# Performance work log

Measured on AMD Instinct MI355X. Metric: run time of the kernel, lower is better.

## Reference

```python
import jax, jax.numpy as jnp
import numpy as np

V, C, BLK = 32000, 512, 2048
B, T = 4, 2048
EPS = 1e-5


def _layernorm(x, g, b):
    mu = jnp.mean(x, axis=-1, keepdims=True)
    var = jnp.mean(jnp.square(x - mu), axis=-1, keepdims=True)
    return (x - mu) * jax.lax.rsqrt(var + EPS) * g + b


def setup_inputs() -> dict:
    key = jax.random.key(0)
    ks = jax.random.split(key, 16)
    s = 0.02
    return {
        "idx": jax.random.randint(ks[0], (B, T), 0, V),
        "targets": jax.random.randint(ks[1], (B, T), 0, V),
        "tok_emb": jax.random.normal(ks[2], (V, C), jnp.float32) * s,
        "pos_emb": jax.random.normal(ks[3], (BLK, C), jnp.float32) * s,
        "Wk": jax.random.normal(ks[4], (C, C), jnp.float32) * s,
        "Wq": jax.random.normal(ks[5], (C, C), jnp.float32) * s,
        "Wv": jax.random.normal(ks[6], (C, C), jnp.float32) * s,
        "W1": jax.random.normal(ks[7], (4 * C, C), jnp.float32) * s,
        "b1": jnp.zeros((4 * C,), jnp.float32),
        "W2": jax.random.normal(ks[8], (C, 4 * C), jnp.float32) * s,
        "b2": jnp.zeros((C,), jnp.float32),
        "g1": jnp.ones((C,), jnp.float32),
        "beta1": jnp.zeros((C,), jnp.float32),
        "g2": jnp.ones((C,), jnp.float32),
        "beta2": jnp.zeros((C,), jnp.float32),
        "Wlm": jax.random.normal(ks[9], (V, C), jnp.float32) * s,
        "blm": jnp.zeros((V,), jnp.float32),
    }


def reference(idx, targets, tok_emb, pos_emb, Wk, Wq, Wv, W1, b1, W2, b2,
              g1, beta1, g2, beta2, Wlm, blm):
    # embeddings
    x = tok_emb[idx] + pos_emb[:T]  # [B,T,C]
    # single-head causal self-attention (dropout = identity, eval mode)
    h = _layernorm(x, g1, beta1)
    q = jnp.einsum('btc,dc->btd', h, Wq)
    k = jnp.einsum('btc,dc->btd', h, Wk)
    v = jnp.einsum('btc,dc->btd', h, Wv)
    wei = jnp.einsum('btd,bsd->bts', q, k) * (C ** -0.5)  # [B,T,T]
    mask = jnp.tril(jnp.ones((T, T), bool))
    wei = jnp.where(mask, wei, -jnp.inf)
    wei = jax.nn.softmax(wei, axis=-1)
    x = x + jnp.einsum('bts,bsd->btd', wei, v)
    # FFN
    h2 = _layernorm(x, g2, beta2)
    ff = jax.nn.relu(jnp.einsum('btc,fc->btf', h2, W1) + b1)
    x = x + jnp.einsum('btf,cf->btc', ff, W2) + b2
    # lm head + cross-entropy
    logits = (jnp.einsum('btc,vc->btv', x, Wlm) + blm).reshape(B * T, V)
    logp = jax.nn.log_softmax(logits, axis=-1)
    loss = -jnp.mean(jnp.take_along_axis(logp, targets.reshape(-1, 1), axis=1))
    return logits, loss
```

## Files before the change

### kernel.cpp

```cpp
#include <hip/hip_runtime.h>

typedef __bf16 bf16;
typedef __bf16 bf16x8 __attribute__((ext_vector_type(8)));
typedef float  f32x4  __attribute__((ext_vector_type(4)));

#define NB 4
#define NT 2048
#define NC 512
#define NV 32000
#define NROWS (NB*NT)
#define NCHUNK 250
#define LNEPS 1e-5f
#define SMEM_B 131072

static __device__ __forceinline__ void load_lds16(const bf16* g, char* l) {
  __builtin_amdgcn_global_load_lds(
      (const __attribute__((address_space(1))) void*)g,
      (__attribute__((address_space(3))) void*)l, 16, 0, 0);
}

static __device__ __forceinline__ void bar() {
  asm volatile("" ::: "memory");
  __builtin_amdgcn_s_barrier();
  asm volatile("" ::: "memory");
}

__global__ __launch_bounds__(256)
void cvt_kernel(const float* __restrict__ in, bf16* __restrict__ out, int n8) {
  long i = (long)blockIdx.x * 256 + threadIdx.x;
  long stride = (long)gridDim.x * 256;
  for (; i < n8; i += stride) {
    const float* p = in + i * 8;
    f32x4 a = *(const f32x4*)p;
    f32x4 b = *(const f32x4*)(p + 4);
    bf16x8 o;
    o[0]=(bf16)a.x; o[1]=(bf16)a.y; o[2]=(bf16)a.z; o[3]=(bf16)a.w;
    o[4]=(bf16)b.x; o[5]=(bf16)b.y; o[6]=(bf16)b.z; o[7]=(bf16)b.w;
    *(bf16x8*)(out + i*8) = o;
  }
}

__global__ __launch_bounds__(64)
void embed_ln_kernel(const int* __restrict__ idx, const float* __restrict__ tok,
                     const float* __restrict__ pos, const float* __restrict__ gw,
                     const float* __restrict__ bw,
                     float* __restrict__ x0, bf16* __restrict__ h1) {
  int row = blockIdx.x;
  int t = row & (NT-1);
  int id = idx[row];
  int lane = threadIdx.x;
  const float* tr = tok + (long)id*NC + lane*8;
  const float* pr = pos + (long)t*NC + lane*8;
  f32x4 a0 = *(const f32x4*)tr, a1 = *(const f32x4*)(tr+4);
  f32x4 p0 = *(const f32x4*)pr, p1 = *(const f32x4*)(pr+4);
  f32x4 r0 = a0 + p0, r1 = a1 + p1;
  float* o = x0 + (long)row*NC + lane*8;
  *(f32x4*)o = r0; *(f32x4*)(o+4) = r1;
  float v[8] = {r0.x,r0.y,r0.z,r0.w,r1.x,r1.y,r1.z,r1.w};
  float s = 0.f;
  #pragma unroll
  for (int j=0;j<8;++j) s += v[j];
  #pragma unroll
  for (int m=32;m>=1;m>>=1) s += __shfl_xor(s, m);
  float mu = s * (1.f/NC);
  float sq = 0.f;
  #pragma unroll
  for (int j=0;j<8;++j) { v[j] -= mu; sq += v[j]*v[j]; }
  #pragma unroll
  for (int m=32;m>=1;m>>=1) sq += __shfl_xor(sq, m);
  float rs = rsqrtf(sq * (1.f/NC) + LNEPS);
  const float* gp = gw + lane*8;
  const float* bp = bw + lane*8;
  f32x4 g0 = *(const f32x4*)gp, g1 = *(const f32x4*)(gp+4);
  f32x4 b0 = *(const f32x4*)bp, b1 = *(const f32x4*)(bp+4);
  float gg[8] = {g0.x,g0.y,g0.z,g0.w,g1.x,g1.y,g1.z,g1.w};
  float bb[8] = {b0.x,b0.y,b0.z,b0.w,b1.x,b1.y,b1.z,b1.w};
  bf16x8 oo;
  #pragma unroll
  for (int j=0;j<8;++j) oo[j] = (bf16)(v[j]*rs*gg[j] + bb[j]);
  *(bf16x8*)(h1 + (long)row*NC + lane*8) = oo;
}

__global__ __launch_bounds__(256)
void transpose_kernel(const bf16* __restrict__ v, long ldv, bf16* __restrict__ vt) {
  __shared__ bf16 tile[64][66];
  int b = blockIdx.z;
  int t0 = blockIdx.x*64, c0 = blockIdx.y*64;
  int tid = threadIdx.x;
  int r = tid >> 2, ch = (tid & 3) * 16;
  const bf16* src = v + ((long)b*NT + t0 + r)*ldv + c0 + ch;
  #pragma unroll
  for (int i=0;i<16;++i) tile[r][ch+i] = src[i];
  __syncthreads();
  bf16x8 o0, o1;
  #pragma unroll
  for (int i=0;i<8;++i) o0[i] = tile[ch+i][r];
  #pragma unroll
  for (int i=0;i<8;++i) o1[i] = tile[ch+8+i][r];
  bf16* dst = vt + ((long)b*NC + c0 + r)*NT + t0 + ch;
  *(bf16x8*)dst = o0;
  *(bf16x8*)(dst+8) = o1;
}

__global__ __launch_bounds__(256)
void softmax_kernel(float* __restrict__ S) {
  const int row = blockIdx.x;
  const int t = row & (NT-1);
  const int tid = threadIdx.x;
  float* sr = S + (long)row*NT;
  bf16* pr = (bf16*)S + (long)row*(2*NT);
  const float scale = 0.044194173824159216f;
  f32x4 v0 = *(const f32x4*)(sr + tid*8);
  f32x4 v1 = *(const f32x4*)(sr + tid*8 + 4);
  float v[8] = {v0.x,v0.y,v0.z,v0.w,v1.x,v1.y,v1.z,v1.w};
  int cb = tid*8;
  float mx = -1e30f;
  #pragma unroll
  for (int j=0;j<8;++j) {
    v[j] = (cb + j <= t) ? v[j]*scale : -1e30f;
    mx = fmaxf(mx, v[j]);
  }
  __shared__ float redm[4];
  #pragma unroll
  for (int m=32;m>=1;m>>=1) mx = fmaxf(mx, __shfl_xor(mx, m));
  if ((tid & 63) == 0) redm[tid>>6] = mx;
  __syncthreads();
  mx = fmaxf(fmaxf(redm[0],redm[1]), fmaxf(redm[2],redm[3]));
  float e[8]; float s = 0.f;
  #pragma unroll
  for (int j=0;j<8;++j) { e[j] = (cb + j <= t) ? __expf(v[j]-mx) : 0.f; s += e[j]; }
  __shared__ float reds[4];
  #pragma unroll
  for (int m=32;m>=1;m>>=1) s += __shfl_xor(s, m);
  if ((tid & 63) == 0) reds[tid>>6] = s;
  __syncthreads();
  s = reds[0]+reds[1]+reds[2]+reds[3];
  float inv = 1.f/s;
  bf16x8 o;
  #pragma unroll
  for (int j=0;j<8;++j) o[j] = (bf16)(e[j]*inv);
  *(bf16x8*)(pr + cb) = o;
}

enum { EPI_F32=0, EPI_BF16=1, EPI_BIAS_RELU_BF16=2, EPI_BIAS_RES_BF16=3, EPI_RES_F32=4 };

template<int EPI, bool CAUSAL=false, bool SWAP=false, bool KCHUNK=false>
__global__ __launch_bounds__(512,2)
void gemm256(const bf16* __restrict__ A, const bf16* __restrict__ B, int nkt,
             long lda, long ldb, long sAb, long sBb,
             float* __restrict__ outf, bf16* __restrict__ outb, long ldo, long sOb,
             const float* __restrict__ bias,
             const float* __restrict__ res, long ldr, long sRb) {
  extern __shared__ char smem[];
  int bn, bm;
  if constexpr (SWAP) { bm = blockIdx.x; bn = blockIdx.y; }
  else               { bn = blockIdx.x; bm = blockIdx.y; }
  const int bz = blockIdx.z;
  if constexpr (CAUSAL) { if (bn > bm) return; }
  int nkt_eff = nkt;
  int bzAB = bz;
  long kOff = 0;
  if constexpr (KCHUNK) {
    int c = bz >> 2; bzAB = bz & 3;
    int lim = (bm+1)*4 - c*8;
    if (lim <= 0) return;
    if (lim < nkt_eff) nkt_eff = lim;
    kOff = (long)c*512;
  }

  const int tid = threadIdx.x;
  const int wid = tid >> 6, lane = tid & 63;
  const int wr = wid >> 2, wc = wid & 3;
  const int l15 = lane & 15, g = lane >> 4;

  const bf16* Ab = A + (long)bzAB*sAb + kOff + (long)bm*256*lda;
  const bf16* Bb = B + (long)bzAB*sBb + kOff + (long)bn*256*ldb;

  const int colsw = 8 * ((tid & 7) ^ ((tid >> 3) & 7));
  const bf16* A0 = Ab + (long)(tid >> 3)*lda + colsw;
  const bf16* B0 = Bb + (long)(tid >> 3)*ldb + colsw;

  auto stage = [&](int ab, int t, int h, int slot) {
    char* dst = smem + slot*65536 + ab*32768 + h*16384 + wid*1024;
    const bf16* s0 = (ab ? B0 : A0) + (long)(h*128)*(ab ? ldb : lda) + (long)t*64;
    load_lds16(s0, dst);
    load_lds16(s0 + 64*(ab ? ldb : lda), dst + 8192);
  };

  const char* sm = smem;
  auto aLoad = [&](int slot, int m, int kk) -> bf16x8 {
    int row = m*16 + l15;
    int b = row*128 + ((kk*64 + g*16) ^ ((row & 7) << 4));
    return *(const bf16x8*)(sm + slot*65536 + wr*16384 + b);
  };
  auto bLoad = [&](int slot, int n, int kk) -> bf16x8 {
    int row = (wc & 1)*64 + n*16 + l15;
    int b = row*128 + ((kk*64 + g*16) ^ ((row & 7) << 4));
    return *(const bf16x8*)(sm + slot*65536 + 32768 + (wc >> 1)*16384 + b);
  };

  f32x4 acc[8][4] = {};

  stage(0, 0, 0, 0);
  stage(0, 0, 1, 0);
  stage(1, 0, 0, 0);
  stage(1, 0, 1, 0);
  stage(0, 1, 0, 1);
  asm volatile("s_waitcnt vmcnt(2)" ::: "memory");
  bar();

  const int niter = nkt_eff >> 1;
  for (int it = 0; it < niter; ++it) {
    const int t0 = 2*it, t1 = 2*it + 1;
    const int tn0 = (t0+2 < nkt_eff) ? t0+2 : nkt_eff-1;
    const int tn1 = (t1+2 < nkt_eff) ? t1+2 : nkt_eff-1;
    bf16x8 a0[4][2], a1[4][2], b0[2][2], b1[2][2];

    #pragma unroll
    for (int m=0;m<4;++m) { a0[m][0]=aLoad(0,m,0); a0[m][1]=aLoad(0,m,1); }
    #pragma unroll
    for (int n=0;n<2;++n) { b0[n][0]=bLoad(0,n,0); b0[n][1]=bLoad(0,n,1); }
    stage(0, t1, 1, 1);
    bar();
    __builtin_amdgcn_s_setprio(1);
    #pragma unroll
    for (int m=0;m<4;++m)
      #pragma unroll
      for (int n=0;n<2;++n) {
        acc[m][n] = __builtin_amdgcn_mfma_f32_16x16x32_bf16(a0[m][0], b0[n][0], acc[m][n],0,0,0);
        acc[m][n] = __builtin_amdgcn_mfma_f32_16x16x32_bf16(a0[m][1], b0[n][1], acc[m][n],0,0,0);
      }
    __builtin_amdgcn_s_setprio(0);
    bar();
    #pragma unroll
    for (int n=0;n<2;++n) { b1[n][0]=bLoad(0,n+2,0); b1[n][1]=bLoad(0,n+2,1); }
    stage(1, t1, 0, 1);
    bar();
    __builtin_amdgcn_s_setprio(1);
    #pragma unroll
    for (int m=0;m<4;++m)
      #pragma unroll
      for (int n=0;n<2;++n) {
        acc[m][n+2] = __builtin_amdgcn_mfma_f32_16x16x32_bf16(a0[m][0], b1[n][0], acc[m][n+2],0,0,0);
        acc[m][n+2] = __builtin_amdgcn_mfma_f32_16x16x32_bf16(a0[m][1], b1[n][1], acc[m][n+2],0,0,0);
      }
    __builtin_amdgcn_s_setprio(0);
    bar();
    #pragma unroll
    for (int m=0;m<4;++m) { a1[m][0]=aLoad(0,m+4,0); a1[m][1]=aLoad(0,m+4,1); }
    stage(1, t1, 1, 1);
    bar();
    __builtin_amdgcn_s_setprio(1);
    #pragma unroll
    for (int m=0;m<4;++m)
      #pragma unroll
      for (int n=0;n<2;++n) {
        acc[m+4][n+2] = __builtin_amdgcn_mfma_f32_16x16x32_bf16(a1[m][0], b1[n][0], acc[m+4][n+2],0,0,0);
        acc[m+4][n+2] = __builtin_amdgcn_mfma_f32_16x16x32_bf16(a1[m][1], b1[n][1], acc[m+4][n+2],0,0,0);
      }
    __builtin_amdgcn_s_setprio(0);
    bar();
    stage(0, tn0, 0, 0);
    asm volatile("s_waitcnt vmcnt(2)" ::: "memory");
    bar();
    __builtin_amdgcn_s_setprio(1);
    #pragma unroll
    for (int m=0;m<4;++m)
      #pragma unroll
      for (int n=0;n<2;++n) {
        acc[m+4][n] = __builtin_amdgcn_mfma_f32_16x16x32_bf16(a1[m][0], b0[n][0], acc[m+4][n],0,0,0);
        acc[m+4][n] = __builtin_amdgcn_mfma_f32_16x16x32_bf16(a1[m][1], b0[n][1], acc[m+4][n],0,0,0);
      }
    __builtin_amdgcn_s_setprio(0);
    bar();
    #pragma unroll
    for (int m=0;m<4;++m) { a0[m][0]=aLoad(1,m,0); a0[m][1]=aLoad(1,m,1); }
    #pragma unroll
    for (int n=0;n<2;++n) { b0[n][0]=bLoad(1,n,0); b0[n][1]=bLoad(1,n,1); }
    stage(0, tn0, 1, 0);
    bar();
    __builtin_amdgcn_s_setprio(1);
    #pragma unroll
    for (int m=0;m<4;++m)
      #pragma unroll
      for (int n=0;n<2;++n) {
        acc[m][n] = __builtin_amdgcn_mfma_f32_16x16x32_bf16(a0[m][0], b0[n][0], acc[m][n],0,0,0);
        acc[m][n] = __builtin_amdgcn_mfma_f32_16x16x32_bf16(a0[m][1], b0[n][1], acc[m][n],0,0,0);
      }
    __builtin_amdgcn_s_setprio(0);
    bar();
    #pragma unroll
    for (int n=0;n<2;++n) { b1[n][0]=bLoad(1,n+2,0); b1[n][1]=bLoad(1,n+2,1); }
    stage(1, tn0, 0, 0);
    bar();
    __builtin_amdgcn_s_setprio(1);
    #pragma unroll
    for (int m=0;m<4;++m)
      #pragma unroll
      for (int n=0;n<2;++n) {
        acc[m][n+2] = __builtin_amdgcn_mfma_f32_16x16x32_bf16(a0[m][0], b1[n][0], acc[m][n+2],0,0,0);
        acc[m][n+2] = __builtin_amdgcn_mfma_f32_16x16x32_bf16(a0[m][1], b1[n][1], acc[m][n+2],0,0,0);
      }
    __builtin_amdgcn_s_setprio(0);
    bar();
    #pragma unroll
    for (int m=0;m<4;++m) { a1[m][0]=aLoad(1,m+4,0); a1[m][1]=aLoad(1,m+4,1); }
    stage(1, tn0, 1, 0);
    bar();
    __builtin_amdgcn_s_setprio(1);
    #pragma unroll
    for (int m=0;m<4;++m)
      #pragma unroll
      for (int n=0;n<2;++n) {
        acc[m+4][n+2] = __builtin_amdgcn_mfma_f32_16x16x32_bf16(a1[m][0], b1[n][0], acc[m+4][n+2],0,0,0);
        acc[m+4][n+2] = __builtin_amdgcn_mfma_f32_16x16x32_bf16(a1[m][1], b1[n][1], acc[m+4][n+2],0,0,0);
      }
    __builtin_amdgcn_s_setprio(0);
    bar();
    stage(0, tn1, 0, 1);
    asm volatile("s_waitcnt vmcnt(2)" ::: "memory");
    bar();
    __builtin_amdgcn_s_setprio(1);
    #pragma unroll
    for (int m=0;m<4;++m)
      #pragma unroll
      for (int n=0;n<2;++n) {
        acc[m+4][n] = __builtin_amdgcn_mfma_f32_16x16x32_bf16(a1[m][0], b0[n][0], acc[m+4][n],0,0,0);
        acc[m+4][n] = __builtin_amdgcn_mfma_f32_16x16x32_bf16(a1[m][1], b0[n][1], acc[m+4][n],0,0,0);
      }
    __builtin_amdgcn_s_setprio(0);
    bar();
  }

  const long rowbase = (long)bm*256 + wr*128;
  const long colbase = (long)bn*256 + wc*64;

  #pragma unroll
  for (int m=0;m<8;++m)
    #pragma unroll
    for (int n=0;n<4;++n) {
      long c = colbase + n*16 + l15;
      #pragma unroll
      for (int q_=0;q_<4;++q_) {
        long rr = rowbase + m*16 + g*4 + q_;
        float v = acc[m][n][q_];
        if constexpr (EPI == EPI_F32) {
          outf[(long)bz*sOb + rr*ldo + c] = v;
        } else if constexpr (EPI == EPI_BF16) {
          outb[(long)bz*sOb + rr*ldo + c] = (bf16)v;
        } else if constexpr (EPI == EPI_BIAS_RELU_BF16) {
          outb[rr*ldo + c] = (bf16)fmaxf(v + bias[c], 0.f);
        } else if constexpr (EPI == EPI_BIAS_RES_BF16) {
          outb[rr*ldo + c] = (bf16)(v + bias[c] + res[rr*ldr + c]);
        } else if constexpr (EPI == EPI_RES_F32) {
          outf[(long)bz*sOb + rr*ldo + c] = v + res[(long)bz*sRb + rr*ldr + c];
        }
      }
    }
}

__global__ __launch_bounds__(256)
void lmhead128(const bf16* __restrict__ A, const bf16* __restrict__ B,
               const float* __restrict__ bias, float* __restrict__ outf,
               float* __restrict__ pmax, float* __restrict__ psum) {
  __shared__ char As[8192];
  __shared__ char Bs[8192];
  const int bm = blockIdx.x, bn = blockIdx.y;
  const int tid = threadIdx.x;
  const int wid = tid >> 6, lane = tid & 63;
  const int wr = wid >> 1, wc = wid & 1;
  const int l15 = lane & 15, g = lane >> 4;

  const int p0 = tid, p1 = tid + 256;
  const int r0_ = 2*(p0>>3) + ((p0>>2)&1), c0_ = 8*((p0&3) ^ ((p0>>3)&3));
  const int r1_ = 2*(p1>>3) + ((p1>>2)&1), c1_ = 8*((p1&3) ^ ((p1>>3)&3));
  const bf16* A00 = A + ((long)bm*128 + r0_)*NC + c0_;
  const bf16* A01 = A + ((long)bm*128 + r1_)*NC + c1_;
  const bf16* B00 = B + ((long)bn*128 + r0_)*NC + c0_;
  const bf16* B01 = B + ((long)bn*128 + r1_)*NC + c1_;
  char* dA0 = As + wid*1024;
  char* dA1 = As + 4096 + wid*1024;
  char* dB0 = Bs + wid*1024;
  char* dB1 = Bs + 4096 + wid*1024;

  f32x4 acc[4][4] = {};

  for (int kt = 0; kt < 16; ++kt) {
    __syncthreads();
    load_lds16(A00 + kt*32, dA0);
    load_lds16(A01 + kt*32, dA1);
    load_lds16(B00 + kt*32, dB0);
    load_lds16(B01 + kt*32, dB1);
    __syncthreads();
    bf16x8 af[4], bf_[4];
    #pragma unroll
    for (int m=0;m<4;++m) {
      int R = wr*64 + m*16 + l15;
      af[m] = *(const bf16x8*)(As + (R>>1)*128 + (R&1)*64 + ((g ^ ((R>>1)&3))<<4));
    }
    #pragma unroll
    for (int n=0;n<4;++n) {
      int R = wc*64 + n*16 + l15;
      bf_[n] = *(const bf16x8*)(Bs + (R>>1)*128 + (R&1)*64 + ((g ^ ((R>>1)&3))<<4));
    }
    #pragma unroll
    for (int m=0;m<4;++m)
      #pragma unroll
      for (int n=0;n<4;++n)
        acc[m][n] = __builtin_amdgcn_mfma_f32_16x16x32_bf16(af[m], bf_[n], acc[m][n],0,0,0);
  }

  const long rowb = (long)bm*128;
  const long colb = (long)bn*128;
  #pragma unroll
  for (int m=0;m<4;++m)
    #pragma unroll
    for (int n=0;n<4;++n) {
      long c = colb + wc*64 + n*16 + l15;
      float bv = bias[c];
      #pragma unroll
      for (int q=0;q<4;++q) {
        acc[m][n][q] += bv;
        long rr = rowb + wr*64 + m*16 + g*4 + q;
        __builtin_nontemporal_store(acc[m][n][q], &outf[rr*NV + c]);
      }
    }
  __syncthreads();
  float* redm = (float*)As;
  float* reds = redm + 256;
  #pragma unroll
  for (int m=0;m<4;++m)
    #pragma unroll
    for (int q=0;q<4;++q) {
      float mx = fmaxf(fmaxf(acc[m][0][q], acc[m][1][q]),
                       fmaxf(acc[m][2][q], acc[m][3][q]));
      #pragma unroll
      for (int msk=8;msk>=1;msk>>=1) mx = fmaxf(mx, __shfl_xor(mx, msk));
      float se = 0.f;
      #pragma unroll
      for (int n=0;n<4;++n) se += __expf(acc[m][n][q] - mx);
      #pragma unroll
      for (int msk=8;msk>=1;msk>>=1) se += __shfl_xor(se, msk);
      if (l15 == 0) {
        int R = wr*64 + m*16 + g*4 + q;
        redm[wc*128 + R] = mx;
        reds[wc*128 + R] = se;
      }
    }
  __syncthreads();
  if (tid < 128) {
    float m0 = redm[tid], m1 = redm[128+tid];
    float M = fmaxf(m0, m1);
    float Sv = reds[tid]*__expf(m0-M) + reds[128+tid]*__expf(m1-M);
    long row = rowb + tid;
    pmax[row*NCHUNK + bn] = M;
    psum[row*NCHUNK + bn] = Sv;
  }
}

__global__ __launch_bounds__(64)
void pv_combine_ln_kernel(const float* __restrict__ part, const float* __restrict__ x0,
                          const float* __restrict__ gw, const float* __restrict__ bw,
                          float* __restrict__ x1, bf16* __restrict__ h2) {
  int row = blockIdx.x;
  int b = row >> 11, t = row & (NT-1);
  int lane = threadIdx.x;
  int nC = (t >> 9) + 1;
  const float* xr = x0 + (long)row*NC + lane*8;
  f32x4 a0 = *(const f32x4*)xr, a1 = *(const f32x4*)(xr+4);
  for (int c = 0; c < nC; ++c) {
    const float* pr = part + ((long)(c*4 + b)*NT + t)*NC + lane*8;
    a0 += *(const f32x4*)pr; a1 += *(const f32x4*)(pr+4);
  }
  float* o = x1 + (long)row*NC + lane*8;
  *(f32x4*)o = a0; *(f32x4*)(o+4) = a1;
  float v[8] = {a0.x,a0.y,a0.z,a0.w,a1.x,a1.y,a1.z,a1.w};
  float s = 0.f;
  #pragma unroll
  for (int j=0;j<8;++j) s += v[j];
  #pragma unroll
  for (int m=32;m>=1;m>>=1) s += __shfl_xor(s, m);
  float mu = s * (1.f/NC);
  float sq = 0.f;
  #pragma unroll
  for (int j=0;j<8;++j) { v[j] -= mu; sq += v[j]*v[j]; }
  #pragma unroll
  for (int m=32;m>=1;m>>=1) sq += __shfl_xor(sq, m);
  float rs = rsqrtf(sq * (1.f/NC) + LNEPS);
  const float* gp = gw + lane*8;
  const float* bp = bw + lane*8;
  f32x4 g0 = *(const f32x4*)gp, g1 = *(const f32x4*)(gp+4);
  f32x4 b0 = *(const f32x4*)bp, b1 = *(const f32x4*)(bp+4);
  float gg[8] = {g0.x,g0.y,g0.z,g0.w,g1.x,g1.y,g1.z,g1.w};
  float bb[8] = {b0.x,b0.y,b0.z,b0.w,b1.x,b1.y,b1.z,b1.w};
  bf16x8 oo;
  #pragma unroll
  for (int j=0;j<8;++j) oo[j] = (bf16)(v[j]*rs*gg[j] + bb[j]);
  *(bf16x8*)(h2 + (long)row*NC + lane*8) = oo;
}

__global__ __launch_bounds__(64)
void ffn2_combine_kernel(const float* __restrict__ part, const float* __restrict__ x1,
                         const float* __restrict__ b2, bf16* __restrict__ x2) {
  int row = blockIdx.x;
  int lane = threadIdx.x;
  const float* xr = x1 + (long)row*NC + lane*8;
  f32x4 a0 = *(const f32x4*)xr, a1 = *(const f32x4*)(xr+4);
  const float* br = b2 + lane*8;
  a0 += *(const f32x4*)br; a1 += *(const f32x4*)(br+4);
  #pragma unroll
  for (int z = 0; z < 4; ++z) {
    const float* pr = part + ((long)z*NROWS + row)*NC + lane*8;
    a0 += *(const f32x4*)pr; a1 += *(const f32x4*)(pr+4);
  }
  bf16x8 o;
  o[0]=(bf16)a0.x; o[1]=(bf16)a0.y; o[2]=(bf16)a0.z; o[3]=(bf16)a0.w;
  o[4]=(bf16)a1.x; o[5]=(bf16)a1.y; o[6]=(bf16)a1.z; o[7]=(bf16)a1.w;
  *(bf16x8*)(x2 + (long)row*NC + lane*8) = o;
}

__global__ __launch_bounds__(256)
void loss1_kernel(const float* __restrict__ pmax, const float* __restrict__ psum,
                  const float* __restrict__ logits, const int* __restrict__ targets,
                  float* __restrict__ rowloss) {
  int row = blockIdx.x;
  int tid = threadIdx.x;
  int lane = tid & 63, wv = tid >> 6;
  float cm = (tid < NCHUNK) ? pmax[(long)row*NCHUNK + tid] : -1e30f;
  float cs = (tid < NCHUNK) ? psum[(long)row*NCHUNK + tid] : 0.f;
  float mx = cm;
  #pragma unroll
  for (int m=32;m>=1;m>>=1) mx = fmaxf(mx, __shfl_xor(mx, m));
  __shared__ float rm[4];
  if (lane == 0) rm[wv] = mx;
  __syncthreads();
  float M = fmaxf(fmaxf(rm[0],rm[1]), fmaxf(rm[2],rm[3]));
  float sc = cs * __expf(cm - M);
  #pragma unroll
  for (int m=32;m>=1;m>>=1) sc += __shfl_xor(sc, m);
  __shared__ float rs_[4];
  if (lane == 0) rs_[wv] = sc;
  __syncthreads();
  if (tid == 0) {
    float Sv = rs_[0]+rs_[1]+rs_[2]+rs_[3];
    float lse = M + logf(Sv);
    int tgt = targets[row];
    float lg = logits[(long)row*NV + tgt];
    rowloss[row] = lse - lg;
  }
}

__global__ __launch_bounds__(256)
void loss2_kernel(const float* __restrict__ rowloss, float* __restrict__ out) {
  int tid = threadIdx.x;
  float s = 0.f;
  for (int i = tid; i < NROWS; i += 256) s += rowloss[i];
  #pragma unroll
  for (int m=32;m>=1;m>>=1) s += __shfl_xor(s, m);
  __shared__ float rs_[4];
  if ((tid & 63) == 0) rs_[tid>>6] = s;
  __syncthreads();
  if (tid == 0) out[0] = (rs_[0]+rs_[1]+rs_[2]+rs_[3]) * (1.f/NROWS);
}

extern "C" void kernel_launch(void* const* d_in, const int* in_sizes, int n_in,
                              void* d_out, int out_size, void* d_ws, size_t ws_size,
                              hipStream_t stream) {
  const int*   idx  = (const int*)d_in[0];
  const int*   tgt  = (const int*)d_in[1];
  const float* tok  = (const float*)d_in[2];
  const float* pos  = (const float*)d_in[3];
  const float* Wk   = (const float*)d_in[4];
  const float* Wq   = (const float*)d_in[5];
  const float* Wv   = (const float*)d_in[6];
  const float* W1   = (const float*)d_in[7];
  const float* b1   = (const float*)d_in[8];
  const float* W2   = (const float*)d_in[9];
  const float* b2   = (const float*)d_in[10];
  const float* g1   = (const float*)d_in[11];
  const float* be1  = (const float*)d_in[12];
  const float* g2   = (const float*)d_in[13];
  const float* be2  = (const float*)d_in[14];
  const float* Wlm  = (const float*)d_in[15];
  const float* blm  = (const float*)d_in[16];

  float* logits = (float*)d_out;
  float* loss   = logits + (long)NROWS*NV;

  char* w = (char*)d_ws;
  auto alloc = [&](size_t bytes) -> char* {
    char* p = w; w += (bytes + 255) & ~(size_t)255; return p;
  };
  bf16* wqkvb = (bf16*)alloc((size_t)3*NC*NC*2);
  bf16* w1b   = (bf16*)alloc((size_t)4*NC*NC*2);
  bf16* w2b   = (bf16*)alloc((size_t)4*NC*NC*2);
  bf16* wlmb  = (bf16*)alloc((size_t)NV*NC*2);
  float* x0   = (float*)alloc((size_t)NROWS*NC*4);
  bf16* h1b   = (bf16*)alloc((size_t)NROWS*NC*2);
  bf16* qkvb  = (bf16*)alloc((size_t)NROWS*3*NC*2);
  bf16* vtb   = (bf16*)alloc((size_t)NROWS*NC*2);
  float* Sb   = (float*)alloc((size_t)NB*NT*NT*4);
  float* pvp  = (float*)alloc((size_t)16*NT*NC*4);
  float* x1   = (float*)alloc((size_t)NROWS*NC*4);
  bf16* h2b   = (bf16*)alloc((size_t)NROWS*NC*2);
  bf16* ffb   = (bf16*)alloc((size_t)NROWS*4*NC*2);
  bf16* x2b   = (bf16*)alloc((size_t)NROWS*NC*2);
  float* pmax = (float*)alloc((size_t)NROWS*NCHUNK*4);
  float* psum = (float*)alloc((size_t)NROWS*NCHUNK*4);
  float* rowloss = (float*)alloc((size_t)NROWS*4);
  float* ff2p = Sb;

  hipFuncSetAttribute((const void*)gemm256<EPI_BF16,false,false,false>,
                      hipFuncAttributeMaxDynamicSharedMemorySize, SMEM_B);
  hipFuncSetAttribute((const void*)gemm256<EPI_F32,true,false,false>,
                      hipFuncAttributeMaxDynamicSharedMemorySize, SMEM_B);
  hipFuncSetAttribute((const void*)gemm256<EPI_F32,false,false,true>,
                      hipFuncAttributeMaxDynamicSharedMemorySize, SMEM_B);
  hipFuncSetAttribute((const void*)gemm256<EPI_F32,false,false,false>,
                      hipFuncAttributeMaxDynamicSharedMemorySize, SMEM_B);
  hipFuncSetAttribute((const void*)gemm256<EPI_BIAS_RELU_BF16,false,true,false>,
                      hipFuncAttributeMaxDynamicSharedMemorySize, SMEM_B);

  auto cvt = [&](const float* in, bf16* out, long n) {
    int n8 = (int)(n/8);
    int blocks = (n8 + 255)/256; if (blocks > 2048) blocks = 2048;
    cvt_kernel<<<blocks, 256, 0, stream>>>(in, out, n8);
  };
  cvt(Wq, wqkvb, (long)NC*NC);
  cvt(Wk, wqkvb + (long)NC*NC, (long)NC*NC);
  cvt(Wv, wqkvb + (long)2*NC*NC, (long)NC*NC);
  cvt(W1, w1b, (long)4*NC*NC);
  cvt(W2, w2b, (long)4*NC*NC);
  cvt(Wlm, wlmb, (long)NV*NC);

  embed_ln_kernel<<<NROWS, 64, 0, stream>>>(idx, tok, pos, g1, be1, x0, h1b);

  gemm256<EPI_BF16><<<dim3(6,32,1), 512, SMEM_B, stream>>>(
      h1b, wqkvb, 8, NC, NC, 0, 0, nullptr, qkvb, 3*NC, 0,
      nullptr, nullptr, 0, 0);

  transpose_kernel<<<dim3(NT/64, NC/64, NB), 256, 0, stream>>>(qkvb + 2*NC, 3*NC, vtb);

  gemm256<EPI_F32,true><<<dim3(8,8,NB), 512, SMEM_B, stream>>>(
      qkvb, qkvb + NC, 8, 3*NC, 3*NC, (long)NT*3*NC, (long)NT*3*NC,
      Sb, nullptr, NT, (long)NT*NT,
      nullptr, nullptr, 0, 0);

  softmax_kernel<<<NROWS, 256, 0, stream>>>(Sb);

  gemm256<EPI_F32,false,false,true><<<dim3(2,8,16), 512, SMEM_B, stream>>>(
      (const bf16*)Sb, vtb, 8, 2*NT, NT, (long)NT*2*NT, (long)NC*NT,
      pvp, nullptr, NC, (long)NT*NC,
      nullptr, nullptr, 0, 0);

  pv_combine_ln_kernel<<<NROWS, 64, 0, stream>>>(pvp, x0, g2, be2, x1, h2b);

  gemm256<EPI_BIAS_RELU_BF16,false,true><<<dim3(32,8,1), 512, SMEM_B, stream>>>(
      h2b, w1b, 8, NC, NC, 0, 0, nullptr, ffb, 4*NC, 0,
      b1, nullptr, 0, 0);

  gemm256<EPI_F32><<<dim3(2,32,4), 512, SMEM_B, stream>>>(
      ffb, w2b, 8, 4*NC, 4*NC, 512, 512,
      ff2p, nullptr, NC, (long)NROWS*NC,
      nullptr, nullptr, 0, 0);

  ffn2_combine_kernel<<<NROWS, 64, 0, stream>>>(ff2p, x1, b2, x2b);

  lmhead128<<<dim3(64, NCHUNK), 256, 0, stream>>>(x2b, wlmb, blm, logits, pmax, psum);

  loss1_kernel<<<NROWS, 256, 0, stream>>>(pmax, psum, logits, tgt, rowloss);
  loss2_kernel<<<1, 256, 0, stream>>>(rowloss, loss);
}
```

Baseline: 756.2 us.

## Double-buffer LM-head GEMM tiles with BK=64 and async LDS prefetch

Rewrites the LM-head GEMM main loop to use two 32KB LDS slots with a K-tile of 64 instead of 32. The next tile is prefetched via global_load_lds while MFMAs run on the current one, and the loop has one barrier per iteration instead of two. MFMA sections also raise wave priority. The cost is 64KB of LDS per block, which may lower occupancy for a kernel that also writes a large fp32 logits output.

```diff
diff --git a/kernel.cpp b/kernel.cpp
--- a/kernel.cpp
+++ b/kernel.cpp
@@ -363,51 +363,67 @@
 void lmhead128(const bf16* __restrict__ A, const bf16* __restrict__ B,
                const float* __restrict__ bias, float* __restrict__ outf,
                float* __restrict__ pmax, float* __restrict__ psum) {
-  __shared__ char As[8192];
-  __shared__ char Bs[8192];
+  __shared__ char sm[65536];
   const int bm = blockIdx.x, bn = blockIdx.y;
   const int tid = threadIdx.x;
   const int wid = tid >> 6, lane = tid & 63;
   const int wr = wid >> 1, wc = wid & 1;
   const int l15 = lane & 15, g = lane >> 4;
 
-  const int p0 = tid, p1 = tid + 256;
-  const int r0_ = 2*(p0>>3) + ((p0>>2)&1), c0_ = 8*((p0&3) ^ ((p0>>3)&3));
-  const int r1_ = 2*(p1>>3) + ((p1>>2)&1), c1_ = 8*((p1&3) ^ ((p1>>3)&3));
-  const bf16* A00 = A + ((long)bm*128 + r0_)*NC + c0_;
-  const bf16* A01 = A + ((long)bm*128 + r1_)*NC + c1_;
-  const bf16* B00 = B + ((long)bn*128 + r0_)*NC + c0_;
-  const bf16* B01 = B + ((long)bn*128 + r1_)*NC + c1_;
-  char* dA0 = As + wid*1024;
-  char* dA1 = As + 4096 + wid*1024;
-  char* dB0 = Bs + wid*1024;
-  char* dB1 = Bs + 4096 + wid*1024;
+  const int rr_ = tid >> 3;
+  const int colsw = 8 * ((tid & 7) ^ (rr_ & 7));
+  const bf16* Abase = A + ((long)bm*128 + rr_)*NC + colsw;
+  const bf16* Bbase = B + ((long)bn*128 + rr_)*NC + colsw;
+
+  auto stage = [&](int kt, int slot) {
+    char* dA = sm + slot*32768 + wid*1024;
+    char* dB = sm + slot*32768 + 16384 + wid*1024;
+    const bf16* a = Abase + kt*64;
+    const bf16* b = Bbase + kt*64;
+    #pragma unroll
+    for (int j = 0; j < 4; ++j) {
+      load_lds16(a + (long)j*32*NC, dA + j*4096);
+      load_lds16(b + (long)j*32*NC, dB + j*4096);
+    }
+  };
+
+  auto aLoad = [&](int slot, int m, int kk) -> bf16x8 {
+    int R = wr*64 + m*16 + l15;
+    int s = kk*4 + g;
+    return *(const bf16x8*)(sm + slot*32768 + R*128 + ((s ^ (R & 7)) << 4));
+  };
+  auto bLoad = [&](int slot, int n, int kk) -> bf16x8 {
+    int R = wc*64 + n*16 + l15;
+    int s = kk*4 + g;
+    return *(const bf16x8*)(sm + slot*32768 + 16384 + R*128 + ((s ^ (R & 7)) << 4));
+  };
 
   f32x4 acc[4][4] = {};
 
-  for (int kt = 0; kt < 16; ++kt) {
-    __syncthreads();
-    load_lds16(A00 + kt*32, dA0);
-    load_lds16(A01 + kt*32, dA1);
-    load_lds16(B00 + kt*32, dB0);
-    load_lds16(B01 + kt*32, dB1);
-    __syncthreads();
-    bf16x8 af[4], bf_[4];
-    #pragma unroll
-    for (int m=0;m<4;++m) {
-      int R = wr*64 + m*16 + l15;
-      af[m] = *(const bf16x8*)(As + (R>>1)*128 + (R&1)*64 + ((g ^ ((R>>1)&3))<<4));
-    }
-    #pragma unroll
-    for (int n=0;n<4;++n) {
-      int R = wc*64 + n*16 + l15;
-      bf_[n] = *(const bf16x8*)(Bs + (R>>1)*128 + (R&1)*64 + ((g ^ ((R>>1)&3))<<4));
-    }
-    #pragma unroll
-    for (int m=0;m<4;++m)
-      #pragma unroll
-      for (int n=0;n<4;++n)
-        acc[m][n] = __builtin_amdgcn_mfma_f32_16x16x32_bf16(af[m], bf_[n], acc[m][n],0,0,0);
+  stage(0, 0);
+  asm volatile("s_waitcnt vmcnt(0)" ::: "memory");
+  bar();
+
+  int cur = 0;
+  for (int kt = 0; kt < 8; ++kt) {
+    if (kt < 7) stage(kt + 1, cur ^ 1);
+    bf16x8 af[4][2], bf_[4][2];
+    #pragma unroll
+    for (int m=0;m<4;++m) { af[m][0]=aLoad(cur,m,0); af[m][1]=aLoad(cur,m,1); }
+    #pragma unroll
+    for (int n=0;n<4;++n) { bf_[n][0]=bLoad(cur,n,0); bf_[n][1]=bLoad(cur,n,1); }
+    __builtin_amdgcn_s_setprio(1);
+    #pragma unroll
+    for (int m=0;m<4;++m)
+      #pragma unroll
+      for (int n=0;n<4;++n) {
+        acc[m][n] = __builtin_amdgcn_mfma_f32_16x16x32_bf16(af[m][0], bf_[n][0], acc[m][n],0,0,0);
+        acc[m][n] = __builtin_amdgcn_mfma_f32_16x16x32_bf16(af[m][1], bf_[n][1], acc[m][n],0,0,0);
+      }
+    __builtin_amdgcn_s_setprio(0);
+    asm volatile("s_waitcnt vmcnt(0)" ::: "memory");
+    bar();
+    cur ^= 1;
   }
 
   const long rowb = (long)bm*128;
@@ -426,7 +442,7 @@
       }
     }
   __syncthreads();
-  float* redm = (float*)As;
+  float* redm = (float*)sm;
   float* reds = redm + 256;
   #pragma unroll
   for (int m=0;m<4;++m)
```

After: 809.5 us. 1.07x slower.

## Double-buffer LM-head LDS loads and write per-wave softmax partials directly

Applied to the files above, without the earlier changes.

The LM-head GEMM kernel now uses two LDS stages, prefetching the next K tile while MFMAs run on the current one, and raises MFMA priority with setprio. It drops the block-level LDS reduction of row max and sum and instead writes per-half-tile partials directly, doubling NCHUNK to 500. The logits store moves after the reduction, and loss1 is widened to 512 threads to combine the extra partials. This trades more partial-sum traffic and 32KB of LDS per block for fewer barriers and overlapped loads in the dominant GEMM.

```diff
diff --git a/kernel.cpp b/kernel.cpp
--- a/kernel.cpp
+++ b/kernel.cpp
@@ -9,7 +9,7 @@
 #define NC 512
 #define NV 32000
 #define NROWS (NB*NT)
-#define NCHUNK 250
+#define NCHUNK 500
 #define LNEPS 1e-5f
 #define SMEM_B 131072
 
@@ -359,12 +359,11 @@
     }
 }
 
-__global__ __launch_bounds__(256)
+__global__ __launch_bounds__(256,4)
 void lmhead128(const bf16* __restrict__ A, const bf16* __restrict__ B,
                const float* __restrict__ bias, float* __restrict__ outf,
                float* __restrict__ pmax, float* __restrict__ psum) {
-  __shared__ char As[8192];
-  __shared__ char Bs[8192];
+  __shared__ char sm[32768];
   const int bm = blockIdx.x, bn = blockIdx.y;
   const int tid = threadIdx.x;
   const int wid = tid >> 6, lane = tid & 63;
@@ -378,56 +377,62 @@
   const bf16* A01 = A + ((long)bm*128 + r1_)*NC + c1_;
   const bf16* B00 = B + ((long)bn*128 + r0_)*NC + c0_;
   const bf16* B01 = B + ((long)bn*128 + r1_)*NC + c1_;
-  char* dA0 = As + wid*1024;
-  char* dA1 = As + 4096 + wid*1024;
-  char* dB0 = Bs + wid*1024;
-  char* dB1 = Bs + 4096 + wid*1024;
+
+  auto stage = [&](int kt, int slot) {
+    char* base = sm + slot*16384 + wid*1024;
+    load_lds16(A00 + kt*32, base);
+    load_lds16(A01 + kt*32, base + 4096);
+    load_lds16(B00 + kt*32, base + 8192);
+    load_lds16(B01 + kt*32, base + 12288);
+  };
+
+  auto aLoad = [&](int slot, int m) -> bf16x8 {
+    int R = wr*64 + m*16 + l15;
+    return *(const bf16x8*)(sm + slot*16384 + (R>>1)*128 + (R&1)*64
+                            + ((g ^ ((R>>1)&3)) << 4));
+  };
+  auto bLoad = [&](int slot, int n) -> bf16x8 {
+    int R = wc*64 + n*16 + l15;
+    return *(const bf16x8*)(sm + slot*16384 + 8192 + (R>>1)*128 + (R&1)*64
+                            + ((g ^ ((R>>1)&3)) << 4));
+  };
 
   f32x4 acc[4][4] = {};
 
+  stage(0, 0);
+  asm volatile("s_waitcnt vmcnt(0)" ::: "memory");
+  bar();
+
+  int cur = 0;
   for (int kt = 0; kt < 16; ++kt) {
-    __syncthreads();
-    load_lds16(A00 + kt*32, dA0);
-    load_lds16(A01 + kt*32, dA1);
-    load_lds16(B00 + kt*32, dB0);
-    load_lds16(B01 + kt*32, dB1);
-    __syncthreads();
+    if (kt < 15) stage(kt + 1, cur ^ 1);
     bf16x8 af[4], bf_[4];
     #pragma unroll
-    for (int m=0;m<4;++m) {
-      int R = wr*64 + m*16 + l15;
-      af[m] = *(const bf16x8*)(As + (R>>1)*128 + (R&1)*64 + ((g ^ ((R>>1)&3))<<4));
-    }
-    #pragma unroll
-    for (int n=0;n<4;++n) {
-      int R = wc*64 + n*16 + l15;
-      bf_[n] = *(const bf16x8*)(Bs + (R>>1)*128 + (R&1)*64 + ((g ^ ((R>>1)&3))<<4));
-    }
+    for (int m=0;m<4;++m) af[m] = aLoad(cur, m);
+    #pragma unroll
+    for (int n=0;n<4;++n) bf_[n] = bLoad(cur, n);
+    __builtin_amdgcn_s_setprio(1);
     #pragma unroll
     for (int m=0;m<4;++m)
       #pragma unroll
       for (int n=0;n<4;++n)
         acc[m][n] = __builtin_amdgcn_mfma_f32_16x16x32_bf16(af[m], bf_[n], acc[m][n],0,0,0);
+    __builtin_amdgcn_s_setprio(0);
+    asm volatile("s_waitcnt vmcnt(0)" ::: "memory");
+    bar();
+    cur ^= 1;
   }
 
   const long rowb = (long)bm*128;
   const long colb = (long)bn*128;
   #pragma unroll
-  for (int m=0;m<4;++m)
-    #pragma unroll
-    for (int n=0;n<4;++n) {
-      long c = colb + wc*64 + n*16 + l15;
-      float bv = bias[c];
-      #pragma unroll
-      for (int q=0;q<4;++q) {
-        acc[m][n][q] += bv;
-        long rr = rowb + wr*64 + m*16 + g*4 + q;
-        __builtin_nontemporal_store(acc[m][n][q], &outf[rr*NV + c]);
-      }
-    }
-  __syncthreads();
-  float* redm = (float*)As;
-  float* reds = redm + 256;
+  for (int n=0;n<4;++n) {
+    float bv = bias[colb + wc*64 + n*16 + l15];
+    #pragma unroll
+    for (int m=0;m<4;++m)
+      #pragma unroll
+      for (int q=0;q<4;++q) acc[m][n][q] += bv;
+  }
   #pragma unroll
   for (int m=0;m<4;++m)
     #pragma unroll
@@ -442,20 +447,22 @@
       #pragma unroll
       for (int msk=8;msk>=1;msk>>=1) se += __shfl_xor(se, msk);
       if (l15 == 0) {
-        int R = wr*64 + m*16 + g*4 + q;
-        redm[wc*128 + R] = mx;
-        reds[wc*128 + R] = se;
+        long row = rowb + wr*64 + m*16 + g*4 + q;
+        pmax[row*NCHUNK + bn*2 + wc] = mx;
+        psum[row*NCHUNK + bn*2 + wc] = se;
       }
     }
-  __syncthreads();
-  if (tid < 128) {
-    float m0 = redm[tid], m1 = redm[128+tid];
-    float M = fmaxf(m0, m1);
-    float Sv = reds[tid]*__expf(m0-M) + reds[128+tid]*__expf(m1-M);
-    long row = rowb + tid;
-    pmax[row*NCHUNK + bn] = M;
-    psum[row*NCHUNK + bn] = Sv;
-  }
+  #pragma unroll
+  for (int m=0;m<4;++m)
+    #pragma unroll
+    for (int n=0;n<4;++n) {
+      long c = colb + wc*64 + n*16 + l15;
+      #pragma unroll
+      for (int q=0;q<4;++q) {
+        long rr = rowb + wr*64 + m*16 + g*4 + q;
+        __builtin_nontemporal_store(acc[m][n][q], &outf[rr*NV + c]);
+      }
+    }
 }
 
 __global__ __launch_bounds__(64)
@@ -519,7 +526,7 @@
   *(bf16x8*)(x2 + (long)row*NC + lane*8) = o;
 }
 
-__global__ __launch_bounds__(256)
+__global__ __launch_bounds__(512)
 void loss1_kernel(const float* __restrict__ pmax, const float* __restrict__ psum,
                   const float* __restrict__ logits, const int* __restrict__ targets,
                   float* __restrict__ rowloss) {
@@ -531,18 +538,22 @@
   float mx = cm;
   #pragma unroll
   for (int m=32;m>=1;m>>=1) mx = fmaxf(mx, __shfl_xor(mx, m));
-  __shared__ float rm[4];
+  __shared__ float rm[8];
   if (lane == 0) rm[wv] = mx;
   __syncthreads();
-  float M = fmaxf(fmaxf(rm[0],rm[1]), fmaxf(rm[2],rm[3]));
+  float M = rm[0];
+  #pragma unroll
+  for (int i=1;i<8;++i) M = fmaxf(M, rm[i]);
   float sc = cs * __expf(cm - M);
   #pragma unroll
   for (int m=32;m>=1;m>>=1) sc += __shfl_xor(sc, m);
-  __shared__ float rs_[4];
+  __shared__ float rs_[8];
   if (lane == 0) rs_[wv] = sc;
   __syncthreads();
   if (tid == 0) {
-    float Sv = rs_[0]+rs_[1]+rs_[2]+rs_[3];
+    float Sv = 0.f;
+    #pragma unroll
+    for (int i=0;i<8;++i) Sv += rs_[i];
     float lse = M + logf(Sv);
     int tgt = targets[row];
     float lg = logits[(long)row*NV + tgt];
@@ -666,8 +677,8 @@
 
   ffn2_combine_kernel<<<NROWS, 64, 0, stream>>>(ff2p, x1, b2, x2b);
 
-  lmhead128<<<dim3(64, NCHUNK), 256, 0, stream>>>(x2b, wlmb, blm, logits, pmax, psum);
-
-  loss1_kernel<<<NROWS, 256, 0, stream>>>(pmax, psum, logits, tgt, rowloss);
+  lmhead128<<<dim3(64, NV/128), 256, 0, stream>>>(x2b, wlmb, blm, logits, pmax, psum);
+
+  loss1_kernel<<<NROWS, 512, 0, stream>>>(pmax, psum, logits, tgt, rowloss);
   loss2_kernel<<<1, 256, 0, stream>>>(rowloss, loss);
 }
```

Result: no change. 742.5 us (-1.8%).
